# Performance work log

Hardware: AMD Instinct MI355X
Metric: run time of the kernel (lower is better)

## Reference

```python
import jax, jax.numpy as jnp
import numpy as np

N_NODES = 100000
N_EDGES = 1000000
F_IN = 5
H = 64
N_LAYERS = 3


def _mlp2(x, w1, b1, w2, b2):
    # Linear -> ReLU -> Linear -> ReLU
    h = jax.nn.relu(x @ w1 + b1)
    return jax.nn.relu(h @ w2 + b2)


def setup_inputs() -> dict:
    key = jax.random.key(0)
    ks = jax.random.split(key, 12)
    s = 0.05
    return {
        "node_features": jax.random.normal(ks[0], (N_NODES, F_IN), jnp.float32),
        "edge_index": jax.random.randint(ks[1], (2, N_EDGES), 0, N_NODES, jnp.int64 if jax.config.jax_enable_x64 else jnp.int32),
        "enc_w1": jax.random.normal(ks[2], (F_IN, H), jnp.float32) * s,
        "enc_b1": jnp.zeros((H,), jnp.float32),
        "enc_w2": jax.random.normal(ks[3], (H, H), jnp.float32) * s,
        "enc_b2": jnp.zeros((H,), jnp.float32),
        "msg_w1": jax.random.normal(ks[4], (N_LAYERS, 2 * H, H), jnp.float32) * s,
        "msg_b1": jnp.zeros((N_LAYERS, H), jnp.float32),
        "msg_w2": jax.random.normal(ks[5], (N_LAYERS, H, H), jnp.float32) * s,
        "msg_b2": jnp.zeros((N_LAYERS, H), jnp.float32),
        "upd_w1": jax.random.normal(ks[6], (N_LAYERS, 2 * H, H), jnp.float32) * s,
        "upd_b1": jnp.zeros((N_LAYERS, H), jnp.float32),
        "upd_w2": jax.random.normal(ks[7], (N_LAYERS, H, H), jnp.float32) * s,
        "upd_b2": jnp.zeros((N_LAYERS, H), jnp.float32),
        "out_w1": jax.random.normal(ks[8], (H, H), jnp.float32) * s,
        "out_b1": jnp.zeros((H,), jnp.float32),
        "out_w2": jax.random.normal(ks[9], (H, 3), jnp.float32) * s,
        "out_b2": jnp.zeros((3,), jnp.float32),
    }


def reference(node_features, edge_index, enc_w1, enc_b1, enc_w2, enc_b2,
              msg_w1, msg_b1, msg_w2, msg_b2,
              upd_w1, upd_b1, upd_w2, upd_b2,
              out_w1, out_b1, out_w2, out_b2):
    n = node_features.shape[0]
    src, dst = edge_index[0], edge_index[1]
    h = _mlp2(node_features, enc_w1, enc_b1, enc_w2, enc_b2)  # [N, H]
    # precompute in-degree counts (constant across layers)
    counts = jax.ops.segment_sum(jnp.ones((src.shape[0],), h.dtype), dst, num_segments=n)
    denom = jnp.maximum(counts, 1.0)[:, None]  # nodes w/o incoming edges -> agg stays zero
    for l in range(N_LAYERS):
        combined = jnp.concatenate([h[src], h[dst]], axis=-1)  # [E, 2H]
        m = _mlp2(combined, msg_w1[l], msg_b1[l], msg_w2[l], msg_b2[l])  # [E, H]
        agg = jax.ops.segment_sum(m, dst, num_segments=n) / denom  # scatter-mean by dst
        h = _mlp2(jnp.concatenate([h, agg], axis=-1), upd_w1[l], upd_b1[l], upd_w2[l], upd_b2[l])
    pred = jax.nn.relu(h @ out_w1 + out_b1) @ out_w2 + out_b2  # [N, 3]
    return 2.0 * jnp.pi * jax.nn.sigmoid(pred)
```

## Files before the change

### kernel.cpp

```cpp
#include <hip/hip_runtime.h>
#include <math.h>

#define NN 100000
#define NE 1000000
#define H 64
#define EB 128
#define MBT 256
#define MSTRIDE 130
#define NSH 8

typedef _Float16 f16x8 __attribute__((ext_vector_type(8)));
typedef _Float16 f16x2 __attribute__((ext_vector_type(2)));
typedef float f32x4  __attribute__((ext_vector_type(4)));

static __device__ __forceinline__ float relu_(float x){ return fmaxf(x, 0.0f); }

static __device__ __forceinline__ unsigned short f2h_(float f){
  union { _Float16 h; unsigned short u; } x; x.h = (_Float16)f; return x.u;
}
static __device__ __forceinline__ float h2f_(unsigned short u){
  union { unsigned short u; _Float16 h; } x; x.u = u; return (float)x.h;
}
static __device__ __forceinline__ unsigned int pkh_(float lo, float hi){
  union { f16x2 v; unsigned int u; } x;
  x.v[0] = (_Float16)lo; x.v[1] = (_Float16)hi;
  return x.u;
}
static __device__ __forceinline__ unsigned int addrelu2_(unsigned int a, unsigned int b){
  union { unsigned int u; f16x2 v; } x, y, r;
  x.u = a; y.u = b;
  f16x2 s = x.v + y.v;
  _Float16 z = (_Float16)0.0f;
  r.v[0] = (s[0] > z) ? s[0] : z;
  r.v[1] = (s[1] > z) ? s[1] : z;
  return r.u;
}
static __device__ __forceinline__ unsigned int mulpk_(unsigned int a, f16x2 s){
  union { unsigned int u; f16x2 v; } x;
  x.u = a; x.v = x.v * s;
  return x.u;
}
static __device__ __forceinline__ void atomic_pk_f16_(unsigned short* p, unsigned int pk){
  asm volatile("global_atomic_pk_add_f16 %0, %1, off" :: "v"(p), "v"(pk) : "memory");
}
static __device__ __forceinline__ void fma32(float* o, float a, const float* wr){
  #pragma unroll
  for (int j=0;j<32;j++) o[j] = fmaf(a, wr[j], o[j]);
}

__global__ __launch_bounds__(256, 2) void enc_full_kernel(
    const float* __restrict__ x,
    const float* __restrict__ w1, const float* __restrict__ b1,
    const float* __restrict__ w2, const float* __restrict__ b2,
    unsigned short* __restrict__ hbf)
{
  int v = blockIdx.x*256 + threadIdx.x;
  if (v >= NN) return;
  float in0[5];
  #pragma unroll
  for (int k=0;k<5;k++) in0[k] = x[(size_t)v*5 + k];
  float o[64];
  #pragma unroll
  for (int j=0;j<64;j++) o[j] = b2[j];
  #pragma unroll 4
  for (int k=0;k<64;k++){
    float tk = b1[k];
    #pragma unroll
    for (int kk=0;kk<5;kk++) tk = fmaf(in0[kk], w1[kk*H + k], tk);
    tk = relu_(tk);
    const float* wr = w2 + k*H;
    #pragma unroll
    for (int j=0;j<64;j++) o[j] = fmaf(tk, wr[j], o[j]);
  }
  unsigned int u[32];
  #pragma unroll
  for (int j=0;j<32;j++) u[j] = pkh_(relu_(o[2*j]), relu_(o[2*j+1]));
  uint4* dp = (uint4*)(hbf + (size_t)v*H);
  #pragma unroll
  for (int j=0;j<8;j++) dp[j] = *(uint4*)&u[4*j];
}

__global__ __launch_bounds__(256) void rank_kernel(const int* __restrict__ dst,
                                                   int* __restrict__ counts8,
                                                   int* __restrict__ rank)
{
  int t = blockIdx.x*256 + threadIdx.x;
  int e0 = t*4;
  int* cs = counts8 + (size_t)(blockIdx.x & (NSH-1))*NN;
  if (e0 + 3 < NE){
    int4 d4 = *(const int4*)(dst + e0);
    int r0 = atomicAdd(&cs[d4.x], 1);
    int r1 = atomicAdd(&cs[d4.y], 1);
    int r2 = atomicAdd(&cs[d4.z], 1);
    int r3 = atomicAdd(&cs[d4.w], 1);
    *(int4*)(rank + e0) = make_int4(r0, r1, r2, r3);
  } else {
    for (int e = e0; e < NE; ++e) rank[e] = atomicAdd(&cs[dst[e]], 1);
  }
}

__global__ __launch_bounds__(1024) void scan1_kernel(const int* __restrict__ counts8,
                                                     int* __restrict__ counts,
                                                     int* __restrict__ pfx,
                                                     int* __restrict__ row_excl,
                                                     int* __restrict__ part)
{
  __shared__ int wsum[16];
  int tid = threadIdx.x;
  int i = blockIdx.x*1024 + tid;
  int v = 0;
  if (i < NN){
    int run = 0;
    #pragma unroll
    for (int sh=0; sh<NSH; sh++){
      int c = counts8[(size_t)sh*NN + i];
      pfx[(size_t)sh*NN + i] = run;
      run += c;
    }
    v = run;
    counts[i] = run;
  }
  int lane = tid & 63, w = tid >> 6;
  int s = v;
  #pragma unroll
  for (int off=1; off<64; off<<=1){
    int t = __shfl_up(s, off, 64);
    if (lane >= off) s += t;
  }
  if (lane == 63) wsum[w] = s;
  __syncthreads();
  if (w == 0 && lane < 16){
    int t = wsum[lane];
    #pragma unroll
    for (int off=1; off<16; off<<=1){
      int u = __shfl_up(t, off, 64);
      if (lane >= off) t += u;
    }
    wsum[lane] = t;
  }
  __syncthreads();
  int base = (w > 0) ? wsum[w-1] : 0;
  int incl = base + s;
  if (i < NN) row_excl[i] = incl - v;
  if (tid == 1023) part[blockIdx.x] = incl;
}

__global__ __launch_bounds__(128) void scan2_kernel(int* __restrict__ part, int nparts)
{
  __shared__ int buf[128];
  int tid = threadIdx.x;
  int v = (tid < nparts) ? part[tid] : 0;
  buf[tid] = v;
  __syncthreads();
  for (int off=1; off<128; off<<=1){
    int t = (tid >= off) ? buf[tid-off] : 0;
    __syncthreads();
    buf[tid] += t;
    __syncthreads();
  }
  if (tid < nparts) part[tid] = buf[tid] - v;
}

__global__ __launch_bounds__(256) void fill_kernel(
    const int* __restrict__ src, const int* __restrict__ dst,
    const int* __restrict__ row_excl, const int* __restrict__ part,
    const int* __restrict__ pfx,
    const int* __restrict__ rank, int2* __restrict__ sedge)
{
  int e = blockIdx.x*256 + threadIdx.x;
  if (e >= NE) return;
  int d = dst[e];
  int sh = (e >> 10) & (NSH-1);
  int p = row_excl[d] + part[d >> 10] + pfx[(size_t)sh*NN + d] + rank[e];
  sedge[p] = make_int2(src[e], d);
}

__global__ __launch_bounds__(256) void count_kernel(const int* __restrict__ dst,
                                                    int* __restrict__ counts)
{
  int e = blockIdx.x*256 + threadIdx.x;
  if (e < NE) atomicAdd(&counts[dst[e]], 1);
}

__global__ __launch_bounds__(256) void prep_all_kernel(
    const float* __restrict__ uw1, const float* __restrict__ uw2,
    const float* __restrict__ mw1, const float* __restrict__ mw2,
    const float* __restrict__ ow1, unsigned short* __restrict__ wp)
{
  int i = blockIdx.x*256 + threadIdx.x;
  if (i >= 77824) return;
  float val;
  if (i < 24576){
    int l = i / 8192, r = i & 8191;
    int j = r & 7, col = (r >> 3) & 63, g = r >> 9;
    int k = (g >> 2)*32 + (g & 3)*8 + j;
    val = uw1[(size_t)l*8192 + k*64 + col];
  } else if (i < 36864){
    int t = i - 24576; int l = t / 4096, r = t & 4095;
    int j = r & 7, col = (r >> 3) & 63, g = r >> 9;
    int k = (g >> 2)*32 + (g & 3)*8 + j;
    val = uw2[(size_t)l*4096 + k*64 + col];
  } else if (i < 61440){
    int t = i - 36864; int l = t / 8192, r = t & 8191;
    int j = r & 7, col = (r >> 3) & 127, g = r >> 10;
    int k = (g >> 2)*32 + (g & 3)*8 + j;
    val = mw1[(size_t)l*8192 + ((col >> 6)*64 + k)*64 + (col & 63)];
  } else if (i < 65536){
    int r = i - 61440;
    int j = r & 7, col = (r >> 3) & 63, g = r >> 9;
    int k = (g >> 2)*32 + (g & 3)*8 + j;
    val = ow1[k*64 + col];
  } else {
    int t = i - 65536; int l = t / 4096, r = t & 4095;
    int j = r & 7, col = (r >> 3) & 63, g = r >> 9;
    int k = (g >> 2)*32 + (g & 3)*8 + j;
    val = mw2[(size_t)l*4096 + k*64 + col];
  }
  wp[i] = f2h_(val);
}

__global__ __launch_bounds__(MBT, 4) void msg_mfma_kernel(
    const unsigned short* __restrict__ P,
    const unsigned short* __restrict__ w2p,
    const float* __restrict__ b2,
    const int2* __restrict__ sedge,
    unsigned short* __restrict__ aggh)
{
  __shared__ unsigned short mlds[64*MSTRIDE];
  __shared__ int2 sdl[EB];
  const int tid  = threadIdx.x;
  const int wave = tid >> 6, lane = tid & 63, quad = lane >> 4, c = lane & 15;

  int bid = blockIdx.x;
  int ng = gridDim.x >> 3;
  int lb = (bid < (ng << 3)) ? ((bid & 7)*ng + (bid >> 3)) : bid;
  const int base = lb*EB;

  if (tid < EB){
    int p = base + tid;
    int2 sv = make_int2(0, -1);
    if (p < NE) sv = sedge[p];
    sdl[tid] = sv;
  }

  f16x8 bfr[4][2];
  #pragma unroll
  for (int n=0;n<4;n++)
    #pragma unroll
    for (int kb=0;kb<2;kb++)
      bfr[n][kb] = *(const f16x8*)(w2p + (((kb*4 + quad)*64 + n*16 + c) << 3));
  float bv[4];
  #pragma unroll
  for (int n=0;n<4;n++) bv[n] = b2[n*16 + c];

  __syncthreads();

  const int ebase = wave*32;
  #pragma unroll
  for (int t=0;t<2;t++){
    int2 sd = sdl[ebase + t*16 + c];
    int s = sd.x;
    int d = sd.y < 0 ? 0 : sd.y;
    const unsigned short* p1 = P + (size_t)s*128 + quad*8;
    const unsigned short* p2 = P + (size_t)d*128 + 64 + quad*8;
    f16x8 af[2];
    #pragma unroll
    for (int kb=0;kb<2;kb++){
      uint4 u1 = *(const uint4*)(p1 + kb*32);
      uint4 u2 = *(const uint4*)(p2 + kb*32);
      union { unsigned int u[4]; f16x8 v; } A;
      A.u[0] = addrelu2_(u1.x, u2.x);
      A.u[1] = addrelu2_(u1.y, u2.y);
      A.u[2] = addrelu2_(u1.z, u2.z);
      A.u[3] = addrelu2_(u1.w, u2.w);
      af[kb] = A.v;
    }

    f32x4 acc4[4];
    #pragma unroll
    for (int n=0;n<4;n++) acc4[n] = (f32x4){0.f, 0.f, 0.f, 0.f};
    #pragma unroll
    for (int n=0;n<4;n++){
      acc4[n] = __builtin_amdgcn_mfma_f32_16x16x32_f16(af[0], bfr[n][0], acc4[n], 0, 0, 0);
      acc4[n] = __builtin_amdgcn_mfma_f32_16x16x32_f16(af[1], bfr[n][1], acc4[n], 0, 0, 0);
    }

    int e0 = ebase + t*16 + quad*4;
    #pragma unroll
    for (int n=0;n<4;n++){
      int ch = n*16 + c;
      float v0 = relu_(acc4[n][0] + bv[n]);
      float v1 = relu_(acc4[n][1] + bv[n]);
      float v2 = relu_(acc4[n][2] + bv[n]);
      float v3 = relu_(acc4[n][3] + bv[n]);
      *(unsigned int*)&mlds[ch*MSTRIDE + e0]     = pkh_(v0, v1);
      *(unsigned int*)&mlds[ch*MSTRIDE + e0 + 2] = pkh_(v2, v3);
    }
  }
  __syncthreads();

  {
    const int g = wave;
    const int ch = lane;
    int dA  = sdl[lane].y;
    int dAm = (lane == 0) ? ~dA : sdl[lane-1].y;
    unsigned long long m0 = __ballot(dA != dAm);
    int dB  = sdl[64+lane].y;
    int dBm = sdl[63+lane].y;
    unsigned long long m1 = __ballot(dB != dBm);

    auto isb = [&](int p)->bool{
      return (p < 64) ? ((m0 >> p) & 1ull) : ((m1 >> (p-64)) & 1ull);
    };
    auto nextb = [&](int p)->int{
      int q = p + 1;
      if (q < 64){
        unsigned long long t = m0 >> q;
        if (t) return q + __builtin_ctzll(t);
        q = 64;
      }
      int off = q - 64;
      if (off < 64){
        unsigned long long t = m1 >> off;
        if (t) return q + __builtin_ctzll(t);
      }
      return EB;
    };

    int r = g*32;
    if (g > 0 && !isb(r)) r = nextb(r);
    const int myEnd = (g+1)*32;
    while (r < myEnd){
      int nb = nextb(r);
      int cur = sdl[r].y;
      float s2 = 0.f;
      for (int rr = r; rr < nb; ++rr)
        s2 += h2f_(mlds[ch*MSTRIDE + rr]);
      if (cur >= 0){
        bool bnd = (r == 0) || (nb == EB);
        if (bnd){
          float other = __shfl_xor(s2, 1);
          if ((ch & 1) == 0){
            unsigned int pk = pkh_(s2, other);
            atomic_pk_f16_(aggh + (size_t)cur*H + ch, pk);
          }
        } else {
          aggh[(size_t)cur*H + ch] = f2h_(s2);
        }
      }
      r = nb;
    }
  }
}

__global__ __launch_bounds__(256) void node_fused_kernel(
    const unsigned short* __restrict__ hbf,
    const unsigned short* __restrict__ aggh, const int* __restrict__ counts,
    const unsigned short* __restrict__ uw1p, const float* __restrict__ ub1,
    const unsigned short* __restrict__ uw2p, const float* __restrict__ ub2,
    const unsigned short* __restrict__ w3p,  const float* __restrict__ b3,
    const float* __restrict__ ow2, const float* __restrict__ ob2,
    unsigned short* __restrict__ hout,
    unsigned short* __restrict__ Pout,
    float* __restrict__ outp,
    int mode)
{
  __shared__ __align__(16) unsigned short act[64*72];
  __shared__ __align__(16) unsigned short pst[64*136];
  const int tid = threadIdx.x, wave = tid >> 6, lane = tid & 63;
  const int quad = lane >> 4, c = lane & 15;
  const int vb = blockIdx.x*64;
  int myv = vb + wave*16 + c;
  int vld = myv < NN ? myv : NN-1;

  if (mode != 2){
    int cntv = counts[vld];
    float invf = (cntv > 0) ? (1.0f / (float)cntv) : 0.0f;
    f16x2 invd2; invd2[0] = (_Float16)invf; invd2[1] = (_Float16)invf;
    f16x8 a1[4];
    a1[0] = *(const f16x8*)(hbf + (size_t)vld*H + quad*8);
    a1[1] = *(const f16x8*)(hbf + (size_t)vld*H + 32 + quad*8);
    #pragma unroll
    for (int kb2=0; kb2<2; kb2++){
      uint4 u = *(const uint4*)(aggh + (size_t)vld*H + kb2*32 + quad*8);
      union { unsigned int u[4]; f16x8 v; } A;
      A.u[0] = mulpk_(u.x, invd2);
      A.u[1] = mulpk_(u.y, invd2);
      A.u[2] = mulpk_(u.z, invd2);
      A.u[3] = mulpk_(u.w, invd2);
      a1[2+kb2] = A.v;
    }
    f32x4 acc1[4];
    #pragma unroll
    for (int n=0;n<4;n++) acc1[n] = (f32x4){0.f,0.f,0.f,0.f};
    #pragma unroll
    for (int n=0;n<4;n++){
      #pragma unroll
      for (int kb=0;kb<4;kb++){
        f16x8 b = *(const f16x8*)(uw1p + (((kb*4 + quad)*64 + n*16 + c) << 3));
        acc1[n] = __builtin_amdgcn_mfma_f32_16x16x32_f16(a1[kb], b, acc1[n], 0, 0, 0);
      }
    }
    #pragma unroll
    for (int n=0;n<4;n++){
      float bb = ub1[n*16 + c];
      #pragma unroll
      for (int r=0;r<4;r++)
        act[(wave*16 + quad*4 + r)*72 + n*16 + c] = f2h_(relu_(acc1[n][r] + bb));
    }

    f16x8 a2[2];
    a2[0] = *(const f16x8*)(act + (wave*16 + c)*72 + quad*8);
    a2[1] = *(const f16x8*)(act + (wave*16 + c)*72 + 32 + quad*8);
    f32x4 acc2[4];
    #pragma unroll
    for (int n=0;n<4;n++) acc2[n] = (f32x4){0.f,0.f,0.f,0.f};
    #pragma unroll
    for (int n=0;n<4;n++){
      #pragma unroll
      for (int kb=0;kb<2;kb++){
        f16x8 b = *(const f16x8*)(uw2p + (((kb*4 + quad)*64 + n*16 + c) << 3));
        acc2[n] = __builtin_amdgcn_mfma_f32_16x16x32_f16(a2[kb], b, acc2[n], 0, 0, 0);
      }
    }
    #pragma unroll
    for (int n=0;n<4;n++){
      float bb = ub2[n*16 + c];
      #pragma unroll
      for (int r=0;r<4;r++)
        act[(wave*16 + quad*4 + r)*72 + n*16 + c] = f2h_(relu_(acc2[n][r] + bb));
    }
  }

  f16x8 a3[2];
  if (mode == 2){
    a3[0] = *(const f16x8*)(hbf + (size_t)vld*H + quad*8);
    a3[1] = *(const f16x8*)(hbf + (size_t)vld*H + 32 + quad*8);
  } else {
    a3[0] = *(const f16x8*)(act + (wave*16 + c)*72 + quad*8);
    a3[1] = *(const f16x8*)(act + (wave*16 + c)*72 + 32 + quad*8);
  }

  if (mode == 1){
    f32x4 acc3[4];
    #pragma unroll
    for (int n=0;n<4;n++) acc3[n] = (f32x4){0.f,0.f,0.f,0.f};
    #pragma unroll
    for (int n=0;n<4;n++){
      #pragma unroll
      for (int kb=0;kb<2;kb++){
        f16x8 b = *(const f16x8*)(w3p + (((kb*4 + quad)*64 + n*16 + c) << 3));
        acc3[n] = __builtin_amdgcn_mfma_f32_16x16x32_f16(a3[kb], b, acc3[n], 0, 0, 0);
      }
    }
    #pragma unroll
    for (int n=0;n<4;n++){
      float bb = b3[n*16 + c];
      #pragma unroll
      for (int r=0;r<4;r++)
        act[(wave*16 + quad*4 + r)*72 + n*16 + c] = f2h_(relu_(acc3[n][r] + bb));
    }
  } else {
    f32x4 acc3[8];
    #pragma unroll
    for (int n=0;n<8;n++) acc3[n] = (f32x4){0.f,0.f,0.f,0.f};
    #pragma unroll
    for (int n=0;n<8;n++){
      #pragma unroll
      for (int kb=0;kb<2;kb++){
        f16x8 b = *(const f16x8*)(w3p + (((kb*4 + quad)*128 + n*16 + c) << 3));
        acc3[n] = __builtin_amdgcn_mfma_f32_16x16x32_f16(a3[kb], b, acc3[n], 0, 0, 0);
      }
    }
    #pragma unroll
    for (int n=0;n<8;n++){
      int ch = n*16 + c;
      float bb = (ch >= 64) ? b3[ch - 64] : 0.0f;
      #pragma unroll
      for (int r=0;r<4;r++)
        pst[(wave*16 + quad*4 + r)*136 + ch] = f2h_(acc3[n][r] + bb);
    }
  }

  __syncthreads();

  if (mode == 0){
    #pragma unroll
    for (int rr=0; rr<2; rr++){
      int idx = tid + rr*256;
      int node = idx >> 3, ko = (idx & 7)*8;
      int v = vb + node;
      if (v < NN) *(uint4*)(hout + (size_t)v*H + ko) = *(const uint4*)(act + node*72 + ko);
    }
  }
  if (mode == 0 || mode == 2){
    #pragma unroll
    for (int rr=0; rr<4; rr++){
      int idx = tid + rr*256;
      int node = idx >> 4, cho = (idx & 15)*8;
      int v = vb + node;
      if (v < NN) *(uint4*)(Pout + (size_t)v*128 + cho) = *(const uint4*)(pst + node*136 + cho);
    }
  }
  if (mode == 1){
    if (tid < 192){
      int node = tid / 3;
      int v = vb + node;
      if (v < NN){
        int cm = tid - node*3;
        float s = ob2[cm];
        #pragma unroll 8
        for (int k=0;k<64;k++)
          s = fmaf(h2f_(act[node*72 + k]), ow2[k*3 + cm], s);
        outp[(size_t)v*3 + cm] = 6.283185307179586f / (1.0f + __expf(-s));
      }
    }
  }
}

__global__ __launch_bounds__(256) void enc_kernel_legacy(
    const float* __restrict__ x,
    const float* __restrict__ w1, const float* __restrict__ b1,
    const float* __restrict__ w2, const float* __restrict__ b2,
    float* __restrict__ h)
{
  int v = blockIdx.x*256 + threadIdx.x;
  if (v >= NN) return;
  float in0[5];
  #pragma unroll
  for (int k=0;k<5;k++) in0[k] = x[v*5+k];
  float hid[H];
  #pragma unroll
  for (int j=0;j<H;j++) hid[j] = b1[j];
  #pragma unroll
  for (int k=0;k<5;k++){
    #pragma unroll
    for (int j=0;j<H;j++) hid[j] = fmaf(in0[k], w1[k*H+j], hid[j]);
  }
  float o[H];
  #pragma unroll
  for (int j=0;j<H;j++) o[j] = b2[j];
  #pragma unroll
  for (int k=0;k<H;k++){
    float hk = relu_(hid[k]);
    #pragma unroll
    for (int j=0;j<H;j++) o[j] = fmaf(hk, w2[k*H+j], o[j]);
  }
  float4* hw = (float4*)(h + (size_t)v*H);
  #pragma unroll
  for (int j4=0;j4<H/4;j4++){
    float4 t;
    t.x = relu_(o[4*j4+0]); t.y = relu_(o[4*j4+1]);
    t.z = relu_(o[4*j4+2]); t.w = relu_(o[4*j4+3]);
    hw[j4] = t;
  }
}

__global__ __launch_bounds__(256) void msg_kernel_atomic(
    const float* __restrict__ h,
    const int* __restrict__ src, const int* __restrict__ dst,
    const float* __restrict__ w1, const float* __restrict__ b1,
    const float* __restrict__ w2, const float* __restrict__ b2,
    float* __restrict__ agg)
{
  int e = blockIdx.x*256 + threadIdx.x;
  if (e >= NE) return;
  int s = src[e], d = dst[e];
  const float4* hs = (const float4*)(h + (size_t)s*H);
  const float4* hd = (const float4*)(h + (size_t)d*H);
  float hid[H];
  #pragma unroll
  for (int j=0;j<H;j++) hid[j] = b1[j];
  #pragma unroll 4
  for (int k4=0;k4<16;k4++){
    float4 a = hs[k4];
    const float* wr = w1 + (size_t)(4*k4)*H;
    #pragma unroll
    for (int j=0;j<H;j++) hid[j] = fmaf(a.x, wr[j], hid[j]);
    #pragma unroll
    for (int j=0;j<H;j++) hid[j] = fmaf(a.y, wr[H+j], hid[j]);
    #pragma unroll
    for (int j=0;j<H;j++) hid[j] = fmaf(a.z, wr[2*H+j], hid[j]);
    #pragma unroll
    for (int j=0;j<H;j++) hid[j] = fmaf(a.w, wr[3*H+j], hid[j]);
  }
  #pragma unroll 4
  for (int k4=0;k4<16;k4++){
    float4 a = hd[k4];
    const float* wr = w1 + (size_t)(64 + 4*k4)*H;
    #pragma unroll
    for (int j=0;j<H;j++) hid[j] = fmaf(a.x, wr[j], hid[j]);
    #pragma unroll
    for (int j=0;j<H;j++) hid[j] = fmaf(a.y, wr[H+j], hid[j]);
    #pragma unroll
    for (int j=0;j<H;j++) hid[j] = fmaf(a.z, wr[2*H+j], hid[j]);
    #pragma unroll
    for (int j=0;j<H;j++) hid[j] = fmaf(a.w, wr[3*H+j], hid[j]);
  }
  float o[H];
  #pragma unroll
  for (int j=0;j<H;j++) o[j] = b2[j];
  #pragma unroll
  for (int k=0;k<H;k++){
    float hk = relu_(hid[k]);
    #pragma unroll
    for (int j=0;j<H;j++) o[j] = fmaf(hk, w2[k*H+j], o[j]);
  }
  float* arow = agg + (size_t)d*H;
  #pragma unroll
  for (int j=0;j<H;j++) atomicAdd(arow + j, relu_(o[j]));
}

__global__ __launch_bounds__(256) void div_kernel(float* __restrict__ agg,
                                                  const int* __restrict__ counts)
{
  int i = blockIdx.x*256 + threadIdx.x;
  if (i >= NN*H/4) return;
  int v = i / (H/4);
  float invd = 1.0f / fmaxf((float)counts[v], 1.0f);
  float4* a = (float4*)agg + i;
  float4 t = *a;
  t.x *= invd; t.y *= invd; t.z *= invd; t.w *= invd;
  *a = t;
}

__global__ __launch_bounds__(256) void upd_kernel_legacy(
    float* __restrict__ h, const float* __restrict__ agg,
    const float* __restrict__ w1, const float* __restrict__ b1,
    const float* __restrict__ w2, const float* __restrict__ b2)
{
  int v = blockIdx.x*256 + threadIdx.x;
  if (v >= NN) return;
  const float4* hv = (const float4*)(h + (size_t)v*H);
  const float4* av = (const float4*)(agg + (size_t)v*H);
  float hid[H];
  #pragma unroll
  for (int j=0;j<H;j++) hid[j] = b1[j];
  #pragma unroll 4
  for (int k4=0;k4<16;k4++){
    float4 a = hv[k4];
    const float* wr = w1 + (size_t)(4*k4)*H;
    #pragma unroll
    for (int j=0;j<H;j++) hid[j] = fmaf(a.x, wr[j], hid[j]);
    #pragma unroll
    for (int j=0;j<H;j++) hid[j] = fmaf(a.y, wr[H+j], hid[j]);
    #pragma unroll
    for (int j=0;j<H;j++) hid[j] = fmaf(a.z, wr[2*H+j], hid[j]);
    #pragma unroll
    for (int j=0;j<H;j++) hid[j] = fmaf(a.w, wr[3*H+j], hid[j]);
  }
  #pragma unroll 4
  for (int k4=0;k4<16;k4++){
    float4 a = av[k4];
    const float* wr = w1 + (size_t)(64 + 4*k4)*H;
    #pragma unroll
    for (int j=0;j<H;j++) hid[j] = fmaf(a.x, wr[j], hid[j]);
    #pragma unroll
    for (int j=0;j<H;j++) hid[j] = fmaf(a.y, wr[H+j], hid[j]);
    #pragma unroll
    for (int j=0;j<H;j++) hid[j] = fmaf(a.z, wr[2*H+j], hid[j]);
    #pragma unroll
    for (int j=0;j<H;j++) hid[j] = fmaf(a.w, wr[3*H+j], hid[j]);
  }
  float o[H];
  #pragma unroll
  for (int j=0;j<H;j++) o[j] = b2[j];
  #pragma unroll
  for (int k=0;k<H;k++){
    float hk = relu_(hid[k]);
    #pragma unroll
    for (int j=0;j<H;j++) o[j] = fmaf(hk, w2[k*H+j], o[j]);
  }
  float4* hw = (float4*)(h + (size_t)v*H);
  #pragma unroll
  for (int j4=0;j4<H/4;j4++){
    float4 t;
    t.x = relu_(o[4*j4+0]); t.y = relu_(o[4*j4+1]);
    t.z = relu_(o[4*j4+2]); t.w = relu_(o[4*j4+3]);
    hw[j4] = t;
  }
}

__global__ __launch_bounds__(256) void out_kernel2(
    const float* __restrict__ h,
    const float* __restrict__ w1, const float* __restrict__ b1,
    const float* __restrict__ w2, const float* __restrict__ b2,
    float* __restrict__ out)
{
  int v = blockIdx.x*256 + threadIdx.x;
  if (v >= NN) return;
  const float4* hv = (const float4*)(h + (size_t)v*H);
  float pr[3] = { b2[0], b2[1], b2[2] };
  #pragma unroll 1
  for (int half=0; half<2; half++){
    float o[32];
    #pragma unroll
    for (int j=0;j<32;j++) o[j] = b1[half*32 + j];
    #pragma unroll 4
    for (int k4=0;k4<16;k4++){
      float4 a = hv[k4];
      const float* wr = w1 + (4*k4)*H + half*32;
      fma32(o, a.x, wr); fma32(o, a.y, wr+H); fma32(o, a.z, wr+2*H); fma32(o, a.w, wr+3*H);
    }
    #pragma unroll
    for (int j=0;j<32;j++){
      float hk = relu_(o[j]);
      int k = half*32 + j;
      pr[0] = fmaf(hk, w2[k*3+0], pr[0]);
      pr[1] = fmaf(hk, w2[k*3+1], pr[1]);
      pr[2] = fmaf(hk, w2[k*3+2], pr[2]);
    }
  }
  #pragma unroll
  for (int c=0;c<3;c++)
    out[(size_t)v*3 + c] = 6.283185307179586f / (1.0f + __expf(-pr[c]));
}


extern "C" void kernel_launch(void* const* d_in, const int* in_sizes, int n_in,
                              void* d_out, int out_size, void* d_ws, size_t ws_size,
                              hipStream_t stream)
{
  const float* x      = (const float*)d_in[0];
  const int*   ei     = (const int*)  d_in[1];
  const float* enc_w1 = (const float*)d_in[2];
  const float* enc_b1 = (const float*)d_in[3];
  const float* enc_w2 = (const float*)d_in[4];
  const float* enc_b2 = (const float*)d_in[5];
  const float* msg_w1 = (const float*)d_in[6];
  const float* msg_b1 = (const float*)d_in[7];
  const float* msg_w2 = (const float*)d_in[8];
  const float* msg_b2 = (const float*)d_in[9];
  const float* upd_w1 = (const float*)d_in[10];
  const float* upd_b1 = (const float*)d_in[11];
  const float* upd_w2 = (const float*)d_in[12];
  const float* upd_b2 = (const float*)d_in[13];
  const float* out_w1 = (const float*)d_in[14];
  const float* out_b1 = (const float*)d_in[15];
  const float* out_w2 = (const float*)d_in[16];
  const float* out_b2 = (const float*)d_in[17];
  float* out = (float*)d_out;

  const int* srcp = ei;
  const int* dstp = ei + NE;

  const int nodeBlocks  = (NN + 255)/256;
  const int edgeBlocks  = (NE + 255)/256;
  const int rankBlocks  = (NE + 1023)/1024;
  const int msgBlocks   = (NE + EB - 1)/EB;
  const int scanBlocks  = (NN + 1023)/1024;
  const int fusedBlocks = (NN + 63)/64;

  char* wp_ = (char*)d_ws;
  auto take = [&wp_](size_t bytes) -> char* {
    char* r = wp_;
    wp_ += (bytes + 255) & ~(size_t)255;
    return r;
  };
  unsigned short* hbf = (unsigned short*)take((size_t)NN*H*sizeof(unsigned short));
  unsigned short* P   = (unsigned short*)take((size_t)NN*128*sizeof(unsigned short));
  unsigned short* aggh= (unsigned short*)take((size_t)NN*H*sizeof(unsigned short));
  int* counts         = (int*)take((size_t)NN*sizeof(int));
  int* counts8        = (int*)take((size_t)NSH*NN*sizeof(int));
  int* pfx            = (int*)take((size_t)NSH*NN*sizeof(int));
  int* row_excl       = (int*)take((size_t)NN*sizeof(int));
  int* part           = (int*)take(1024);
  int* rank           = (int*)take((size_t)NE*sizeof(int));
  int2* sedge         = (int2*)take((size_t)NE*sizeof(int2));
  unsigned short* wpz = (unsigned short*)take((size_t)77824*sizeof(unsigned short));
  size_t need = (size_t)(wp_ - (char*)d_ws);

  const size_t UW1 = 0, UW2 = 24576, PPJ = 36864, OW1 = 61440, MW2 = 65536;

  if (ws_size >= need) {
    (void)hipMemsetAsync(counts8, 0, (size_t)NSH*NN*sizeof(int), stream);

    enc_full_kernel<<<nodeBlocks, 256, 0, stream>>>(x, enc_w1, enc_b1, enc_w2, enc_b2, hbf);

    rank_kernel<<<rankBlocks, 256, 0, stream>>>(dstp, counts8, rank);
    scan1_kernel<<<scanBlocks, 1024, 0, stream>>>(counts8, counts, pfx, row_excl, part);
    scan2_kernel<<<1, 128, 0, stream>>>(part, scanBlocks);
    fill_kernel<<<edgeBlocks, 256, 0, stream>>>(srcp, dstp, row_excl, part, pfx, rank, sedge);
    prep_all_kernel<<<(77824 + 255)/256, 256, 0, stream>>>(upd_w1, upd_w2, msg_w1, msg_w2, out_w1, wpz);

    node_fused_kernel<<<fusedBlocks, 256, 0, stream>>>(
        hbf, aggh, counts,
        nullptr, nullptr, nullptr, nullptr,
        wpz + PPJ, msg_b1, nullptr, nullptr,
        nullptr, P, nullptr, 2);

    for (int l=0; l<3; l++){
      (void)hipMemsetAsync(aggh, 0, (size_t)NN*H*sizeof(unsigned short), stream);
      msg_mfma_kernel<<<msgBlocks, MBT, 0, stream>>>(P, wpz + MW2 + (size_t)l*4096,
          msg_b2 + (size_t)l*H, sedge, aggh);
      if (l < 2){
        node_fused_kernel<<<fusedBlocks, 256, 0, stream>>>(
            hbf, aggh, counts,
            wpz + UW1 + (size_t)l*8192, upd_b1 + (size_t)l*H,
            wpz + UW2 + (size_t)l*4096, upd_b2 + (size_t)l*H,
            wpz + PPJ + (size_t)(l+1)*8192, msg_b1 + (size_t)(l+1)*H,
            nullptr, nullptr,
            hbf, P, nullptr, 0);
      } else {
        node_fused_kernel<<<fusedBlocks, 256, 0, stream>>>(
            hbf, aggh, counts,
            wpz + UW1 + (size_t)l*8192, upd_b1 + (size_t)l*H,
            wpz + UW2 + (size_t)l*4096, upd_b2 + (size_t)l*H,
            wpz + OW1, out_b1,
            out_w2, out_b2,
            nullptr, nullptr, out, 1);
      }
    }
  } else {
    char* fp = (char*)d_ws;
    float* fh   = (float*)fp;  fp += (size_t)NN*H*sizeof(float);
    float* fagg = (float*)fp;  fp += (size_t)NN*H*sizeof(float);
    int* fcnt   = (int*)fp;

    (void)hipMemsetAsync(fcnt, 0, NN*sizeof(int), stream);
    enc_kernel_legacy<<<nodeBlocks, 256, 0, stream>>>(x, enc_w1, enc_b1, enc_w2, enc_b2, fh);
    count_kernel<<<edgeBlocks, 256, 0, stream>>>(dstp, fcnt);
    for (int l=0; l<3; l++){
      (void)hipMemsetAsync(fagg, 0, (size_t)NN*H*sizeof(float), stream);
      msg_kernel_atomic<<<edgeBlocks, 256, 0, stream>>>(fh, srcp, dstp,
          msg_w1 + (size_t)l*128*H, msg_b1 + (size_t)l*H,
          msg_w2 + (size_t)l*H*H,   msg_b2 + (size_t)l*H, fagg);
      div_kernel<<<(NN*H/4 + 255)/256, 256, 0, stream>>>(fagg, fcnt);
      upd_kernel_legacy<<<nodeBlocks, 256, 0, stream>>>(fh, fagg,
          upd_w1 + (size_t)l*128*H, upd_b1 + (size_t)l*H,
          upd_w2 + (size_t)l*H*H,   upd_b2 + (size_t)l*H);
    }
    out_kernel2<<<nodeBlocks, 256, 0, stream>>>(fh, out_w1, out_b1, out_w2, out_b2, out);
  }
}
```

Before: 375.4 us.

## Shrink node kernel to one wave per block and merge aggregation memsets

The fused node kernel now runs one 64-lane wave over 16 nodes per block instead of four waves over 64 nodes. This gives more, smaller blocks with less shared memory each, and adds block barriers around the shared staging buffer. The three per-layer memsets of the aggregation buffer are replaced by three separate per-layer buffers placed next to the counts8 buffer and zeroed by one combined memset. That removes launch and serialization overhead at the cost of three times the aggregation workspace.

```diff
diff --git a/kernel.cpp b/kernel.cpp
--- a/kernel.cpp
+++ b/kernel.cpp
@@ -353,7 +353,7 @@
   }
 }
 
-__global__ __launch_bounds__(256) void node_fused_kernel(
+__global__ __launch_bounds__(64) void node_fused_kernel(
     const unsigned short* __restrict__ hbf,
     const unsigned short* __restrict__ aggh, const int* __restrict__ counts,
     const unsigned short* __restrict__ uw1p, const float* __restrict__ ub1,
@@ -365,12 +365,12 @@
     float* __restrict__ outp,
     int mode)
 {
-  __shared__ __align__(16) unsigned short act[64*72];
-  __shared__ __align__(16) unsigned short pst[64*136];
-  const int tid = threadIdx.x, wave = tid >> 6, lane = tid & 63;
+  __shared__ __align__(16) unsigned short act[16*72];
+  __shared__ __align__(16) unsigned short pst[16*136];
+  const int lane = threadIdx.x;
   const int quad = lane >> 4, c = lane & 15;
-  const int vb = blockIdx.x*64;
-  int myv = vb + wave*16 + c;
+  const int vb = blockIdx.x*16;
+  int myv = vb + c;
   int vld = myv < NN ? myv : NN-1;
 
   if (mode != 2){
@@ -406,12 +406,13 @@
       float bb = ub1[n*16 + c];
       #pragma unroll
       for (int r=0;r<4;r++)
-        act[(wave*16 + quad*4 + r)*72 + n*16 + c] = f2h_(relu_(acc1[n][r] + bb));
-    }
+        act[(quad*4 + r)*72 + n*16 + c] = f2h_(relu_(acc1[n][r] + bb));
+    }
+    __syncthreads();
 
     f16x8 a2[2];
-    a2[0] = *(const f16x8*)(act + (wave*16 + c)*72 + quad*8);
-    a2[1] = *(const f16x8*)(act + (wave*16 + c)*72 + 32 + quad*8);
+    a2[0] = *(const f16x8*)(act + c*72 + quad*8);
+    a2[1] = *(const f16x8*)(act + c*72 + 32 + quad*8);
     f32x4 acc2[4];
     #pragma unroll
     for (int n=0;n<4;n++) acc2[n] = (f32x4){0.f,0.f,0.f,0.f};
@@ -423,13 +424,15 @@
         acc2[n] = __builtin_amdgcn_mfma_f32_16x16x32_f16(a2[kb], b, acc2[n], 0, 0, 0);
       }
     }
+    __syncthreads();
     #pragma unroll
     for (int n=0;n<4;n++){
       float bb = ub2[n*16 + c];
       #pragma unroll
       for (int r=0;r<4;r++)
-        act[(wave*16 + quad*4 + r)*72 + n*16 + c] = f2h_(relu_(acc2[n][r] + bb));
-    }
+        act[(quad*4 + r)*72 + n*16 + c] = f2h_(relu_(acc2[n][r] + bb));
+    }
+    __syncthreads();
   }
 
   f16x8 a3[2];
@@ -437,8 +440,8 @@
     a3[0] = *(const f16x8*)(hbf + (size_t)vld*H + quad*8);
     a3[1] = *(const f16x8*)(hbf + (size_t)vld*H + 32 + quad*8);
   } else {
-    a3[0] = *(const f16x8*)(act + (wave*16 + c)*72 + quad*8);
-    a3[1] = *(const f16x8*)(act + (wave*16 + c)*72 + 32 + quad*8);
+    a3[0] = *(const f16x8*)(act + c*72 + quad*8);
+    a3[1] = *(const f16x8*)(act + c*72 + 32 + quad*8);
   }
 
   if (mode == 1){
@@ -453,12 +456,13 @@
         acc3[n] = __builtin_amdgcn_mfma_f32_16x16x32_f16(a3[kb], b, acc3[n], 0, 0, 0);
       }
     }
+    __syncthreads();
     #pragma unroll
     for (int n=0;n<4;n++){
       float bb = b3[n*16 + c];
       #pragma unroll
       for (int r=0;r<4;r++)
-        act[(wave*16 + quad*4 + r)*72 + n*16 + c] = f2h_(relu_(acc3[n][r] + bb));
+        act[(quad*4 + r)*72 + n*16 + c] = f2h_(relu_(acc3[n][r] + bb));
     }
   } else {
     f32x4 acc3[8];
@@ -478,7 +482,7 @@
       float bb = (ch >= 64) ? b3[ch - 64] : 0.0f;
       #pragma unroll
       for (int r=0;r<4;r++)
-        pst[(wave*16 + quad*4 + r)*136 + ch] = f2h_(acc3[n][r] + bb);
+        pst[(quad*4 + r)*136 + ch] = f2h_(acc3[n][r] + bb);
     }
   }
 
@@ -487,7 +491,7 @@
   if (mode == 0){
     #pragma unroll
     for (int rr=0; rr<2; rr++){
-      int idx = tid + rr*256;
+      int idx = lane + rr*64;
       int node = idx >> 3, ko = (idx & 7)*8;
       int v = vb + node;
       if (v < NN) *(uint4*)(hout + (size_t)v*H + ko) = *(const uint4*)(act + node*72 + ko);
@@ -496,18 +500,18 @@
   if (mode == 0 || mode == 2){
     #pragma unroll
     for (int rr=0; rr<4; rr++){
-      int idx = tid + rr*256;
+      int idx = lane + rr*64;
       int node = idx >> 4, cho = (idx & 15)*8;
       int v = vb + node;
       if (v < NN) *(uint4*)(Pout + (size_t)v*128 + cho) = *(const uint4*)(pst + node*136 + cho);
     }
   }
   if (mode == 1){
-    if (tid < 192){
-      int node = tid / 3;
+    if (lane < 48){
+      int node = lane / 3;
       int v = vb + node;
       if (v < NN){
-        int cm = tid - node*3;
+        int cm = lane - node*3;
         float s = ob2[cm];
         #pragma unroll 8
         for (int k=0;k<64;k++)
@@ -749,7 +753,7 @@
   const int rankBlocks  = (NE + 1023)/1024;
   const int msgBlocks   = (NE + EB - 1)/EB;
   const int scanBlocks  = (NN + 1023)/1024;
-  const int fusedBlocks = (NN + 63)/64;
+  const int fusedBlocks = (NN + 15)/16;
 
   char* wp_ = (char*)d_ws;
   auto take = [&wp_](size_t bytes) -> char* {
@@ -759,9 +763,9 @@
   };
   unsigned short* hbf = (unsigned short*)take((size_t)NN*H*sizeof(unsigned short));
   unsigned short* P   = (unsigned short*)take((size_t)NN*128*sizeof(unsigned short));
-  unsigned short* aggh= (unsigned short*)take((size_t)NN*H*sizeof(unsigned short));
   int* counts         = (int*)take((size_t)NN*sizeof(int));
   int* counts8        = (int*)take((size_t)NSH*NN*sizeof(int));
+  unsigned short* aggh3 = (unsigned short*)take((size_t)3*NN*H*sizeof(unsigned short));
   int* pfx            = (int*)take((size_t)NSH*NN*sizeof(int));
   int* row_excl       = (int*)take((size_t)NN*sizeof(int));
   int* part           = (int*)take(1024);
@@ -773,7 +777,8 @@
   const size_t UW1 = 0, UW2 = 24576, PPJ = 36864, OW1 = 61440, MW2 = 65536;
 
   if (ws_size >= need) {
-    (void)hipMemsetAsync(counts8, 0, (size_t)NSH*NN*sizeof(int), stream);
+    (void)hipMemsetAsync(counts8, 0,
+        (size_t)NSH*NN*sizeof(int) + (size_t)3*NN*H*sizeof(unsigned short), stream);
 
     enc_full_kernel<<<nodeBlocks, 256, 0, stream>>>(x, enc_w1, enc_b1, enc_w2, enc_b2, hbf);
 
@@ -783,27 +788,27 @@
     fill_kernel<<<edgeBlocks, 256, 0, stream>>>(srcp, dstp, row_excl, part, pfx, rank, sedge);
     prep_all_kernel<<<(77824 + 255)/256, 256, 0, stream>>>(upd_w1, upd_w2, msg_w1, msg_w2, out_w1, wpz);
 
-    node_fused_kernel<<<fusedBlocks, 256, 0, stream>>>(
-        hbf, aggh, counts,
+    node_fused_kernel<<<fusedBlocks, 64, 0, stream>>>(
+        hbf, aggh3, counts,
         nullptr, nullptr, nullptr, nullptr,
         wpz + PPJ, msg_b1, nullptr, nullptr,
         nullptr, P, nullptr, 2);
 
     for (int l=0; l<3; l++){
-      (void)hipMemsetAsync(aggh, 0, (size_t)NN*H*sizeof(unsigned short), stream);
+      unsigned short* agghl = aggh3 + (size_t)l*NN*H;
       msg_mfma_kernel<<<msgBlocks, MBT, 0, stream>>>(P, wpz + MW2 + (size_t)l*4096,
-          msg_b2 + (size_t)l*H, sedge, aggh);
+          msg_b2 + (size_t)l*H, sedge, agghl);
       if (l < 2){
-        node_fused_kernel<<<fusedBlocks, 256, 0, stream>>>(
-            hbf, aggh, counts,
+        node_fused_kernel<<<fusedBlocks, 64, 0, stream>>>(
+            hbf, agghl, counts,
             wpz + UW1 + (size_t)l*8192, upd_b1 + (size_t)l*H,
             wpz + UW2 + (size_t)l*4096, upd_b2 + (size_t)l*H,
             wpz + PPJ + (size_t)(l+1)*8192, msg_b1 + (size_t)(l+1)*H,
             nullptr, nullptr,
             hbf, P, nullptr, 0);
       } else {
-        node_fused_kernel<<<fusedBlocks, 256, 0, stream>>>(
-            hbf, aggh, counts,
+        node_fused_kernel<<<fusedBlocks, 64, 0, stream>>>(
+            hbf, agghl, counts,
             wpz + UW1 + (size_t)l*8192, upd_b1 + (size_t)l*H,
             wpz + UW2 + (size_t)l*4096, upd_b2 + (size_t)l*H,
             wpz + OW1, out_b1,
```

After: 366.8 us. 2.3% less time.
